# Performance work log

Measured on AMD Instinct MI355X. Metric: run time of the kernel, lower is better.

Reference implementation:

```python
import jax, jax.numpy as jnp
import numpy as np

N_NODES = 50000
N_EDGES = 800000
HID = 128


def setup_inputs() -> dict:
    key = jax.random.key(0)
    ks = jax.random.split(key, 8)
    h = jax.random.normal(ks[0], (N_NODES, HID), dtype=jnp.float32)
    edge_index = jax.random.randint(ks[1], (2, N_EDGES), 0, N_NODES, dtype=jnp.int64)
    edge_attr = jax.random.normal(ks[2], (N_EDGES, HID), dtype=jnp.float32)
    # MLP params: Linear(3H -> H), Linear(H -> 1). Stored as [in, out] so y = x @ W + b.
    s1 = 1.0 / np.sqrt(3 * HID)
    W1 = jax.random.uniform(ks[3], (3 * HID, HID), minval=-s1, maxval=s1, dtype=jnp.float32)
    b1 = jax.random.uniform(ks[4], (HID,), minval=-s1, maxval=s1, dtype=jnp.float32)
    s2 = 1.0 / np.sqrt(HID)
    W2 = jax.random.uniform(ks[5], (HID, 1), minval=-s2, maxval=s2, dtype=jnp.float32)
    b2 = jax.random.uniform(ks[6], (1,), minval=-s2, maxval=s2, dtype=jnp.float32)
    return {"h": h, "edge_index": edge_index, "edge_attr": edge_attr,
            "W1": W1, "b1": b1, "W2": W2, "b2": b2}


def reference(h, edge_index, edge_attr, W1, b1, W2, b2):
    row, col = edge_index[0], edge_index[1]
    h_i = h[row]                      # [E, H] gather of source nodes
    h_j = h[col]                      # [E, H] gather of target nodes
    # Split first Linear over the concat [h_i, h_j, edge_attr] to avoid a [E, 3H] buffer.
    Wa, Wb, Wc = W1[:HID], W1[HID:2 * HID], W1[2 * HID:]
    pre = h_i @ Wa + h_j @ Wb + edge_attr @ Wc + b1      # [E, H]
    a = jax.nn.elu(pre) @ W2 + b2                        # [E, 1]
    a = jax.nn.leaky_relu(a, negative_slope=0.2)
    alpha = jax.nn.softmax(a, axis=0)                    # softmax over all edges (dim=0)
    h_agg = jnp.zeros_like(h).at[row].add(alpha * h_j)   # scatter-add weighted neighbors
    return h_agg
```

## Files before the change

### kernel.cpp

```cpp
#include <hip/hip_runtime.h>
#include <hip/hip_bf16.h>
#include <math.h>

#define NNODES 50000
#define NEDGES 800000
#define HID    128
#define NB_SCAN 196
#define NB_EDGE 6250

typedef short bf16x8 __attribute__((ext_vector_type(8)));
typedef float f32x4  __attribute__((ext_vector_type(4)));

__device__ __forceinline__ unsigned short bf16_rn(float x) {
    union { float f; unsigned int u; } v; v.f = x;
    unsigned int r = v.u + 0x7fffu + ((v.u >> 16) & 1u);
    return (unsigned short)(r >> 16);
}
__device__ __forceinline__ float bf16_to_f(unsigned short u) {
    union { unsigned int u; float f; } v; v.u = ((unsigned int)u) << 16;
    return v.f;
}

__global__ void k_prep(const float* __restrict__ W1, unsigned short* __restrict__ Wt)
{
    const float* Wc = W1 + 256 * 128;
    int base = (blockIdx.x * 256 + threadIdx.x) * 4;
#pragma unroll
    for (int i = 0; i < 4; ++i) {
        int idx = base + i;
        int c = idx >> 7, k = idx & 127;
        Wt[c * 128 + k] = bf16_rn(Wc[k * 128 + c]);
    }
}

__global__ __launch_bounds__(256) void k_gemm_node(
    const float* __restrict__ h, const float* __restrict__ W1,
    const float* __restrict__ b1, unsigned short* __restrict__ Hab)
{
    __shared__ float at[32][132];
    __shared__ float bt[32][128];

    const int tid = threadIdx.x;
    const int tx  = tid & 15;
    const int ty  = tid >> 4;
    const int nb  = blockIdx.x * 128;
    const int by  = blockIdx.y;
    const float* W = W1 + by * 128 * 128;

    float acc[8][8];
#pragma unroll
    for (int j = 0; j < 8; ++j)
#pragma unroll
        for (int c = 0; c < 8; ++c) acc[j][c] = 0.0f;

    for (int ks = 0; ks < 128; ks += 32) {
#pragma unroll
        for (int p = 0; p < 16; ++p) {
            int i  = (tid >> 5) + p * 8;
            int kk = tid & 31;
            int n  = nb + i;
            at[kk][i] = (n < NNODES) ? h[n * 128 + ks + kk] : 0.0f;
        }
#pragma unroll
        for (int p = 0; p < 16; ++p) {
            int kk = (tid >> 7) + p * 2;
            int c  = tid & 127;
            bt[kk][c] = W[(ks + kk) * 128 + c];
        }
        __syncthreads();
#pragma unroll
        for (int k = 0; k < 32; ++k) {
            float av[8], bv[8];
            *(float4*)&av[0] = *(const float4*)&at[k][ty * 8];
            *(float4*)&av[4] = *(const float4*)&at[k][ty * 8 + 4];
            *(float4*)&bv[0] = *(const float4*)&bt[k][tx * 8];
            *(float4*)&bv[4] = *(const float4*)&bt[k][tx * 8 + 4];
#pragma unroll
            for (int j = 0; j < 8; ++j)
#pragma unroll
                for (int c = 0; c < 8; ++c)
                    acc[j][c] = fmaf(av[j], bv[c], acc[j][c]);
        }
        __syncthreads();
    }

    float b1v[8];
    if (by == 0) {
        *(float4*)&b1v[0] = *(const float4*)&b1[tx * 8];
        *(float4*)&b1v[4] = *(const float4*)&b1[tx * 8 + 4];
    } else {
#pragma unroll
        for (int c = 0; c < 8; ++c) b1v[c] = 0.0f;
    }
#pragma unroll
    for (int j = 0; j < 8; ++j) {
        int n = nb + ty * 8 + j;
        if (n < NNODES) {
            unsigned short o[8];
#pragma unroll
            for (int c = 0; c < 8; ++c) o[c] = bf16_rn(acc[j][c] + b1v[c]);
            unsigned short* dst = Hab + (size_t)n * 256 + by * 128 + tx * 8;
            *(int4*)dst = *(int4*)&o[0];
        }
    }
}

__global__ __launch_bounds__(256) void k_edge_mfma(
    const float* __restrict__ ea, const int* __restrict__ eidx,
    const unsigned short* __restrict__ Wt, const float* __restrict__ W2,
    const float* __restrict__ b2, const unsigned short* __restrict__ Hab,
    float* __restrict__ a_out, int* __restrict__ hist,
    float* __restrict__ bmax, float* __restrict__ bsumE)
{
    const int tid  = threadIdx.x;
    const int w    = tid >> 6;
    const int l    = tid & 63;
    const int quad = l >> 4;
    const int lm   = l & 15;
    const int wm   = w * 32;
    const int ebase = blockIdx.x * 128;

    __shared__ float sred[8];

    f32x4 acc[2][8] = {};

    int rows0[4], cols0[4], rows1[4], cols1[4];
    {
        const int e40 = ebase + wm + quad * 4;
        const int e41 = e40 + 16;
#pragma unroll
        for (int r = 0; r < 4; ++r) {
            rows0[r] = eidx[e40 + r];
            cols0[r] = eidx[NEDGES + e40 + r];
            rows1[r] = eidx[e41 + r];
            cols1[r] = eidx[NEDGES + e41 + r];
        }
    }
    if (lm == 0) {
#pragma unroll
        for (int r = 0; r < 4; ++r) {
            atomicAdd(&hist[rows0[r]], 1);
            atomicAdd(&hist[rows1[r]], 1);
        }
    }

    const float* abase0 = ea + (size_t)(ebase + wm + lm) * 128 + quad * 8;
    const float* abase1 = abase0 + 16 * 128;
    float4 raw[2][2][2];
    raw[0][0][0] = *(const float4*)(abase0);
    raw[0][0][1] = *(const float4*)(abase0 + 4);
    raw[0][1][0] = *(const float4*)(abase1);
    raw[0][1][1] = *(const float4*)(abase1 + 4);

#pragma unroll
    for (int stage = 0; stage < 4; ++stage) {
        const int ks  = stage * 32;
        const int cur = stage & 1, nxt = cur ^ 1;
        if (stage < 3) {
            const int ko = ks + 32;
            raw[nxt][0][0] = *(const float4*)(abase0 + ko);
            raw[nxt][0][1] = *(const float4*)(abase0 + ko + 4);
            raw[nxt][1][0] = *(const float4*)(abase1 + ko);
            raw[nxt][1][1] = *(const float4*)(abase1 + ko + 4);
        }
        bf16x8 bfrag[8];
#pragma unroll
        for (int nt = 0; nt < 8; ++nt) {
            const unsigned short* bp = Wt + (lm * 8 + nt) * 128 + ks + quad * 8;
            bfrag[nt] = *(const bf16x8*)bp;
        }
        bf16x8 afrag[2];
#pragma unroll
        for (int mt = 0; mt < 2; ++mt) {
            float4 x0 = raw[cur][mt][0];
            float4 x1 = raw[cur][mt][1];
            bf16x8 f;
            f[0] = (short)bf16_rn(x0.x); f[1] = (short)bf16_rn(x0.y);
            f[2] = (short)bf16_rn(x0.z); f[3] = (short)bf16_rn(x0.w);
            f[4] = (short)bf16_rn(x1.x); f[5] = (short)bf16_rn(x1.y);
            f[6] = (short)bf16_rn(x1.z); f[7] = (short)bf16_rn(x1.w);
            afrag[mt] = f;
        }
#pragma unroll
        for (int mt = 0; mt < 2; ++mt)
#pragma unroll
            for (int nt = 0; nt < 8; ++nt)
                acc[mt][nt] = __builtin_amdgcn_mfma_f32_16x16x32_bf16(
                    afrag[mt], bfrag[nt], acc[mt][nt], 0, 0, 0);
    }

    float w2v[8];
    *(float4*)&w2v[0] = *(const float4*)&W2[lm * 8];
    *(float4*)&w2v[4] = *(const float4*)&W2[lm * 8 + 4];
    const float b2s = b2[0];

    float avl[2] = { -INFINITY, -INFINITY };

#pragma unroll
    for (int mt = 0; mt < 2; ++mt) {
        const int e4 = ebase + wm + mt * 16 + quad * 4;

        bf16x8 hav[4], hbv[4];
#pragma unroll
        for (int r = 0; r < 4; ++r) {
            int row  = (mt == 0) ? rows0[r] : rows1[r];
            int colj = (mt == 0) ? cols0[r] : cols1[r];
            hav[r] = *(const bf16x8*)(Hab + (size_t)row  * 256 + lm * 8);
            hbv[r] = *(const bf16x8*)(Hab + (size_t)colj * 256 + 128 + lm * 8);
        }

        float s0 = 0.f, s1 = 0.f, s2 = 0.f, s3 = 0.f;
#pragma unroll
        for (int r = 0; r < 4; ++r) {
            float sr = 0.f;
#pragma unroll
            for (int nt = 0; nt < 8; ++nt) {
                float ha  = bf16_to_f((unsigned short)hav[r][nt]);
                float hb  = bf16_to_f((unsigned short)hbv[r][nt]);
                float pre = acc[mt][nt][r] + ha + hb;
                float el  = pre > 0.f ? pre : expm1f(pre);
                sr = fmaf(el, w2v[nt], sr);
            }
            if (r == 0) s0 = sr; else if (r == 1) s1 = sr; else if (r == 2) s2 = sr; else s3 = sr;
        }
#pragma unroll
        for (int m = 1; m < 16; m <<= 1) {
            s0 += __shfl_xor(s0, m, 64);
            s1 += __shfl_xor(s1, m, 64);
            s2 += __shfl_xor(s2, m, 64);
            s3 += __shfl_xor(s3, m, 64);
        }
        if (lm < 4) {
            float sum = (lm == 0) ? s0 : (lm == 1) ? s1 : (lm == 2) ? s2 : s3;
            sum += b2s;
            float av = sum >= 0.f ? sum : 0.2f * sum;
            a_out[e4 + lm] = av;
            avl[mt] = av;
        }
    }

    float m = fmaxf(avl[0], avl[1]);
#pragma unroll
    for (int msk = 1; msk < 64; msk <<= 1) m = fmaxf(m, __shfl_xor(m, msk, 64));
    if (l == 0) sred[w] = m;
    __syncthreads();
    float mb = fmaxf(fmaxf(sred[0], sred[1]), fmaxf(sred[2], sred[3]));
    float es = 0.f;
    if (avl[0] > -INFINITY)
        es = expf(avl[0] - mb) + expf(avl[1] - mb);
#pragma unroll
    for (int msk = 1; msk < 64; msk <<= 1) es += __shfl_xor(es, msk, 64);
    if (l == 0) sred[4 + w] = es;
    __syncthreads();
    if (tid == 0) {
        bmax[blockIdx.x]  = mb;
        bsumE[blockIdx.x] = sred[4] + sred[5] + sred[6] + sred[7];
    }
}

__global__ void k_scan_blk(const int* __restrict__ hist, int* __restrict__ offsets,
                           int* __restrict__ bsum)
{
    __shared__ int sd[256];
    int t = threadIdx.x, i = blockIdx.x * 256 + t;
    int v = (i < NNODES) ? hist[i] : 0;
    sd[t] = v; __syncthreads();
    for (int off = 1; off < 256; off <<= 1) {
        int add = (t >= off) ? sd[t - off] : 0;
        __syncthreads();
        sd[t] += add;
        __syncthreads();
    }
    if (i < NNODES) offsets[i] = sd[t] - v;
    if (t == 255) bsum[blockIdx.x] = sd[255];
}

__global__ void k_scan_top(const int* __restrict__ bsum, int* __restrict__ bpre,
                           int* __restrict__ offsets)
{
    __shared__ int sd[256];
    int t = threadIdx.x;
    int v = (t < NB_SCAN) ? bsum[t] : 0;
    sd[t] = v; __syncthreads();
    for (int off = 1; off < 256; off <<= 1) {
        int add = (t >= off) ? sd[t - off] : 0;
        __syncthreads();
        sd[t] += add;
        __syncthreads();
    }
    if (t < NB_SCAN) bpre[t] = sd[t] - v;
    if (t == 255) offsets[NNODES] = sd[255];
}

__global__ void k_scan_add(int* __restrict__ offsets, const int* __restrict__ bpre)
{
    int i = blockIdx.x * 256 + threadIdx.x;
    if (i < NNODES) offsets[i] += bpre[i >> 8];
}

__global__ void k_scatter(const int* __restrict__ eidx, const int* __restrict__ offsets,
                          int* __restrict__ cursor, int2* __restrict__ pairs)
{
    int e = blockIdx.x * 256 + threadIdx.x;
    if (e < NEDGES) {
        int r   = eidx[e];
        int pos = offsets[r] + atomicAdd(&cursor[r], 1);
        pairs[pos] = make_int2(e, eidx[NEDGES + e]);
    }
}

__global__ __launch_bounds__(1024) void k_final(
    const float* __restrict__ bmax, const float* __restrict__ bsumE,
    float* __restrict__ mz)
{
    __shared__ float sd[1024];
    int tid = threadIdx.x;
    float m = -INFINITY;
    for (int i = tid; i < NB_EDGE; i += 1024) m = fmaxf(m, bmax[i]);
    sd[tid] = m; __syncthreads();
    for (int off = 512; off > 0; off >>= 1) {
        if (tid < off) sd[tid] = fmaxf(sd[tid], sd[tid + off]);
        __syncthreads();
    }
    float M = sd[0];
    __syncthreads();
    float s = 0.f;
    for (int i = tid; i < NB_EDGE; i += 1024) s += bsumE[i] * expf(bmax[i] - M);
    sd[tid] = s; __syncthreads();
    for (int off = 512; off > 0; off >>= 1) {
        if (tid < off) sd[tid] += sd[tid + off];
        __syncthreads();
    }
    if (tid == 0) { mz[0] = M; mz[1] = 1.0f / sd[0]; }
}

__global__ void k_alpha(const float* __restrict__ a, const float* __restrict__ mz,
                        int2* __restrict__ pairs)
{
    int i = blockIdx.x * 256 + threadIdx.x;
    if (i < NEDGES) {
        int2 p = pairs[i];
        float al = expf(a[p.x] - mz[0]) * mz[1];
        p.x = __float_as_int(al);
        pairs[i] = p;
    }
}

__global__ __launch_bounds__(256) void k_agg(
    const float* __restrict__ h, const int2* __restrict__ pairs,
    const int* __restrict__ offsets, float* __restrict__ out)
{
    int node = blockIdx.x * 4 + (threadIdx.x >> 6);
    int lane = threadIdx.x & 63;
    if (node >= NNODES) return;
    int s0 = offsets[node], s1 = offsets[node + 1];
    float2 acc = make_float2(0.0f, 0.0f);
    int i = s0;
    for (; i + 8 <= s1; i += 8) {
        int2 p[8];
#pragma unroll
        for (int r = 0; r < 8; ++r) p[r] = pairs[i + r];
        float2 hv[8];
#pragma unroll
        for (int r = 0; r < 8; ++r)
            hv[r] = *(const float2*)(h + (size_t)p[r].y * 128 + lane * 2);
#pragma unroll
        for (int r = 0; r < 8; ++r) {
            float al = __int_as_float(p[r].x);
            acc.x = fmaf(al, hv[r].x, acc.x);
            acc.y = fmaf(al, hv[r].y, acc.y);
        }
    }
    for (; i < s1; ++i) {
        int2 p = pairs[i];
        float al = __int_as_float(p.x);
        float2 hj = *(const float2*)(h + (size_t)p.y * 128 + lane * 2);
        acc.x = fmaf(al, hj.x, acc.x);
        acc.y = fmaf(al, hj.y, acc.y);
    }
    *(float2*)(out + (size_t)node * 128 + lane * 2) = acc;
}

extern "C" void kernel_launch(void* const* d_in, const int* in_sizes, int n_in,
                              void* d_out, int out_size, void* d_ws, size_t ws_size,
                              hipStream_t stream)
{
    const float* h    = (const float*)d_in[0];
    const int*   eidx = (const int*)d_in[1];
    const float* ea   = (const float*)d_in[2];
    const float* W1   = (const float*)d_in[3];
    const float* b1   = (const float*)d_in[4];
    const float* W2   = (const float*)d_in[5];
    const float* b2   = (const float*)d_in[6];
    float* out = (float*)d_out;

    char* ws = (char*)d_ws;
    unsigned short* Hab = (unsigned short*)(ws);
    float* a_arr   = (float*)(ws + 25600000);
    int2*  pairs   = (int2*) (ws + 28800000);
    int*   offsets = (int*)  (ws + 35200000);
    int*   cursor  = (int*)  (ws + 35400192);
    float* bmax    = (float*)(ws + 35600384);
    float* bsumE   = (float*)(ws + 35625984);
    float* mz      = (float*)(ws + 35651584);
    unsigned short* Wt = (unsigned short*)(ws + 35651648);
    int*   bsum_s  = (int*)  (ws + 35684416);
    int*   bpre_s  = (int*)  (ws + 35685440);

    hipMemsetAsync(cursor, 0, NNODES * sizeof(int), stream);

    k_prep<<<16, 256, 0, stream>>>(W1, Wt);
    k_gemm_node<<<dim3((NNODES + 127) / 128, 2), 256, 0, stream>>>(h, W1, b1, Hab);

    k_edge_mfma<<<NB_EDGE, 256, 0, stream>>>(ea, eidx, Wt, W2, b2, Hab,
                                             a_arr, cursor, bmax, bsumE);

    k_scan_blk<<<NB_SCAN, 256, 0, stream>>>(cursor, offsets, bsum_s);
    k_scan_top<<<1, 256, 0, stream>>>(bsum_s, bpre_s, offsets);
    k_scan_add<<<NB_SCAN, 256, 0, stream>>>(offsets, bpre_s);
    hipMemsetAsync(cursor, 0, NNODES * sizeof(int), stream);
    k_scatter<<<(NEDGES + 255) / 256, 256, 0, stream>>>(eidx, offsets, cursor, pairs);

    k_final<<<1, 1024, 0, stream>>>(bmax, bsumE, mz);
    k_alpha<<<(NEDGES + 255) / 256, 256, 0, stream>>>(a_arr, mz, pairs);
    k_agg<<<(NNODES + 3) / 4, 256, 0, stream>>>(h, pairs, offsets, out);
}
```

Baseline: 876.2 us.

## Fuse alpha computation into aggregation, prefetch node gathers, use fast expm1

Removes the separate k_alpha kernel and computes the softmax weight inside k_agg from the raw logit array and the max/normalizer. This saves a launch and one read-write pass over the pairs array. In exchange, each of the 64 lanes per node recomputes expf and performs an extra gather from a. The edge kernel now issues the Hab row and column gathers during the last MFMA stage so their latency overlaps the matrix math, at the cost of more live registers. expm1f is replaced by a polynomial for small magnitudes and __expf-1 otherwise, which may slightly change accuracy.

```diff
diff --git a/kernel.cpp b/kernel.cpp
--- a/kernel.cpp
+++ b/kernel.cpp
@@ -19,6 +19,19 @@
 __device__ __forceinline__ float bf16_to_f(unsigned short u) {
     union { unsigned int u; float f; } v; v.u = ((unsigned int)u) << 16;
     return v.f;
+}
+
+__device__ __forceinline__ float expm1_fast(float x) {
+    float t = 1.9841270e-4f;
+    t = fmaf(t, x, 1.3888889e-3f);
+    t = fmaf(t, x, 8.3333333e-3f);
+    t = fmaf(t, x, 4.1666668e-2f);
+    t = fmaf(t, x, 0.16666667f);
+    t = fmaf(t, x, 0.5f);
+    t = fmaf(t, x, 1.0f);
+    float poly = x * t;
+    float ex   = __expf(x) - 1.0f;
+    return (x > -0.25f) ? poly : ex;
 }
 
 __global__ void k_prep(const float* __restrict__ W1, unsigned short* __restrict__ Wt)
@@ -151,6 +164,8 @@
     raw[0][0][1] = *(const float4*)(abase0 + 4);
     raw[0][1][0] = *(const float4*)(abase1);
     raw[0][1][1] = *(const float4*)(abase1 + 4);
+
+    bf16x8 hav[2][4], hbv[2][4];
 
 #pragma unroll
     for (int stage = 0; stage < 4; ++stage) {
@@ -163,6 +178,15 @@
             raw[nxt][1][0] = *(const float4*)(abase1 + ko);
             raw[nxt][1][1] = *(const float4*)(abase1 + ko + 4);
         }
+        if (stage == 3) {
+#pragma unroll
+            for (int r = 0; r < 4; ++r) {
+                hav[0][r] = *(const bf16x8*)(Hab + (size_t)rows0[r] * 256 + lm * 8);
+                hbv[0][r] = *(const bf16x8*)(Hab + (size_t)cols0[r] * 256 + 128 + lm * 8);
+                hav[1][r] = *(const bf16x8*)(Hab + (size_t)rows1[r] * 256 + lm * 8);
+                hbv[1][r] = *(const bf16x8*)(Hab + (size_t)cols1[r] * 256 + 128 + lm * 8);
+            }
+        }
         bf16x8 bfrag[8];
 #pragma unroll
         for (int nt = 0; nt < 8; ++nt) {
@@ -200,25 +224,16 @@
     for (int mt = 0; mt < 2; ++mt) {
         const int e4 = ebase + wm + mt * 16 + quad * 4;
 
-        bf16x8 hav[4], hbv[4];
-#pragma unroll
-        for (int r = 0; r < 4; ++r) {
-            int row  = (mt == 0) ? rows0[r] : rows1[r];
-            int colj = (mt == 0) ? cols0[r] : cols1[r];
-            hav[r] = *(const bf16x8*)(Hab + (size_t)row  * 256 + lm * 8);
-            hbv[r] = *(const bf16x8*)(Hab + (size_t)colj * 256 + 128 + lm * 8);
-        }
-
         float s0 = 0.f, s1 = 0.f, s2 = 0.f, s3 = 0.f;
 #pragma unroll
         for (int r = 0; r < 4; ++r) {
             float sr = 0.f;
 #pragma unroll
             for (int nt = 0; nt < 8; ++nt) {
-                float ha  = bf16_to_f((unsigned short)hav[r][nt]);
-                float hb  = bf16_to_f((unsigned short)hbv[r][nt]);
+                float ha  = bf16_to_f((unsigned short)hav[mt][r][nt]);
+                float hb  = bf16_to_f((unsigned short)hbv[mt][r][nt]);
                 float pre = acc[mt][nt][r] + ha + hb;
-                float el  = pre > 0.f ? pre : expm1f(pre);
+                float el  = pre > 0.f ? pre : expm1_fast(pre);
                 sr = fmaf(el, w2v[nt], sr);
             }
             if (r == 0) s0 = sr; else if (r == 1) s1 = sr; else if (r == 2) s2 = sr; else s3 = sr;
@@ -334,25 +349,16 @@
     if (tid == 0) { mz[0] = M; mz[1] = 1.0f / sd[0]; }
 }
 
-__global__ void k_alpha(const float* __restrict__ a, const float* __restrict__ mz,
-                        int2* __restrict__ pairs)
-{
-    int i = blockIdx.x * 256 + threadIdx.x;
-    if (i < NEDGES) {
-        int2 p = pairs[i];
-        float al = expf(a[p.x] - mz[0]) * mz[1];
-        p.x = __float_as_int(al);
-        pairs[i] = p;
-    }
-}
-
 __global__ __launch_bounds__(256) void k_agg(
-    const float* __restrict__ h, const int2* __restrict__ pairs,
-    const int* __restrict__ offsets, float* __restrict__ out)
+    const float* __restrict__ h, const float* __restrict__ a,
+    const int2* __restrict__ pairs, const int* __restrict__ offsets,
+    const float* __restrict__ mz, float* __restrict__ out)
 {
     int node = blockIdx.x * 4 + (threadIdx.x >> 6);
     int lane = threadIdx.x & 63;
     if (node >= NNODES) return;
+    const float M    = mz[0];
+    const float invS = mz[1];
     int s0 = offsets[node], s1 = offsets[node + 1];
     float2 acc = make_float2(0.0f, 0.0f);
     int i = s0;
@@ -360,20 +366,23 @@
         int2 p[8];
 #pragma unroll
         for (int r = 0; r < 8; ++r) p[r] = pairs[i + r];
+        float av[8];
+#pragma unroll
+        for (int r = 0; r < 8; ++r) av[r] = a[p[r].x];
         float2 hv[8];
 #pragma unroll
         for (int r = 0; r < 8; ++r)
             hv[r] = *(const float2*)(h + (size_t)p[r].y * 128 + lane * 2);
 #pragma unroll
         for (int r = 0; r < 8; ++r) {
-            float al = __int_as_float(p[r].x);
+            float al = expf(av[r] - M) * invS;
             acc.x = fmaf(al, hv[r].x, acc.x);
             acc.y = fmaf(al, hv[r].y, acc.y);
         }
     }
     for (; i < s1; ++i) {
         int2 p = pairs[i];
-        float al = __int_as_float(p.x);
+        float al = expf(a[p.x] - M) * invS;
         float2 hj = *(const float2*)(h + (size_t)p.y * 128 + lane * 2);
         acc.x = fmaf(al, hj.x, acc.x);
         acc.y = fmaf(al, hj.y, acc.y);
@@ -422,6 +431,5 @@
     k_scatter<<<(NEDGES + 255) / 256, 256, 0, stream>>>(eidx, offsets, cursor, pairs);
 
     k_final<<<1, 1024, 0, stream>>>(bmax, bsumE, mz);
-    k_alpha<<<(NEDGES + 255) / 256, 256, 0, stream>>>(a_arr, mz, pairs);
-    k_agg<<<(NNODES + 3) / 4, 256, 0, stream>>>(h, pairs, offsets, out);
-}
+    k_agg<<<(NNODES + 3) / 4, 256, 0, stream>>>(h, a_arr, pairs, offsets, mz, out);
+}
```

After: 869.2 us. Within noise of the previous version (-0.8%).
